# Performance work log

Hardware: AMD Instinct MI355X
Metric: run time of the kernel (lower is better)

Reference implementation:

```python
import jax, jax.numpy as jnp
import numpy as np

N_NODES = 20000
N_EDGES = 320000
BATCH = 8
N_OBS = 6
N_FIXED = 10
HID = 128
N_LAYERS = 3


def setup_inputs() -> dict:
    key = jax.random.key(0)
    ks = jax.random.split(key, 6)
    x = jax.random.normal(ks[0], (BATCH * N_NODES, N_OBS), dtype=jnp.float32)
    fixed_node_features = jax.random.normal(ks[1], (N_NODES, N_FIXED), dtype=jnp.float32)
    edge_index = jax.random.randint(ks[2], (2, N_EDGES), 0, N_NODES)
    W_in = jax.random.normal(ks[3], (N_OBS + N_FIXED, HID), dtype=jnp.float32) * 0.1
    b_in = jnp.zeros((HID,), jnp.float32)
    Wg = jax.random.normal(ks[4], (N_LAYERS, HID, HID), dtype=jnp.float32) * 0.05
    bg = jnp.zeros((N_LAYERS, HID), jnp.float32)
    return {"x": x, "fixed_node_features": fixed_node_features, "W_in": W_in,
            "b_in": b_in, "Wg": Wg, "bg": bg, "edge_index": edge_index}


def reference(x, fixed_node_features, W_in, b_in, Wg, bg, edge_index):
    # GCN normalization with self-loops (PyG gcn_norm defaults):
    self_loops = jnp.arange(N_NODES)
    row = jnp.concatenate([edge_index[0], self_loops])  # source nodes [E+N]
    col = jnp.concatenate([edge_index[1], self_loops])  # target nodes [E+N]
    deg = jax.ops.segment_sum(jnp.ones_like(col, dtype=jnp.float32), col,
                              num_segments=N_NODES)
    dinv = jnp.where(deg > 0, jax.lax.rsqrt(jnp.maximum(deg, 1.0)), 0.0)
    norm = dinv[row] * dinv[col]  # [E+N]

    # input projection: [B*N, n_obs] -> [B, N, n_obs+n_fixed] -> [B, N, H]
    h = x.reshape(BATCH, N_NODES, N_OBS)
    h = jnp.concatenate(
        [h, jnp.broadcast_to(fixed_node_features, (BATCH, N_NODES, N_FIXED))],
        axis=-1)
    h = h @ W_in + b_in

    # stacked GCNConv + ReLU (gather -> normalize -> scatter-add)
    for l in range(N_LAYERS):
        t = h @ Wg[l]                              # [B, N, H]
        msgs = t[:, row, :] * norm[None, :, None]  # [B, E+N, H]
        agg = jnp.zeros_like(t).at[:, col, :].add(msgs)
        h = jax.nn.relu(agg + bg[l])

    return h.reshape(-1, HID)
```

## Files before the change

kernel.cpp:

```cpp
#include <hip/hip_runtime.h>
#include <hip/hip_bf16.h>
#include <cstdint>

#define N_NODES 20000
#define N_EDGES 320000
#define BATCH 8
#define HID 128

static constexpr size_t O_DEG  = 0;
static constexpr size_t O_CUR  = 81920;
static constexpr size_t O_OFF  = 163840;
static constexpr size_t O_DINV = 245760;
static constexpr size_t O_CSR  = 327680;
static constexpr size_t O_CSRW = 1376256;
static constexpr size_t O_P32  = 3473408;
static constexpr size_t O_HBUF = 3553408;


__global__ void count_deg(const int* __restrict__ col, int* __restrict__ deg) {
    int e = blockIdx.x * 256 + threadIdx.x;
    if (e < N_EDGES) atomicAdd(&deg[col[e]], 1);
}

__global__ void compute_dinv(const int* __restrict__ deg, float* __restrict__ dinv) {
    int i = blockIdx.x * 256 + threadIdx.x;
    if (i < N_NODES) {
        float d = (float)(deg[i] + 1);
        dinv[i] = 1.0f / sqrtf(d);
    }
}

__global__ __launch_bounds__(1024) void scan_offsets(const int* __restrict__ deg,
                                                     int* __restrict__ off) {
    __shared__ int part[1024];
    const int CH = 20;
    int tid = threadIdx.x;
    int base = tid * CH;
    int s = 0;
    for (int i = 0; i < CH; ++i) {
        int idx = base + i;
        if (idx < N_NODES) s += (deg[idx] + 7) & ~7;
    }
    part[tid] = s;
    __syncthreads();
    for (int d = 1; d < 1024; d <<= 1) {
        int add = 0;
        if (tid >= d) add = part[tid - d];
        __syncthreads();
        part[tid] += add;
        __syncthreads();
    }
    int run = part[tid] - s;
    for (int i = 0; i < CH; ++i) {
        int idx = base + i;
        if (idx < N_NODES) {
            off[idx] = run;
            run += (deg[idx] + 7) & ~7;
        }
    }
    if (tid == 1023) off[N_NODES] = part[1023];
}

__global__ void fill_csr(const int* __restrict__ rowi, const int* __restrict__ coli,
                         const float* __restrict__ dinv, const int* __restrict__ off,
                         int* __restrict__ cursor, uint16_t* __restrict__ csr,
                         float* __restrict__ csrw) {
    int e = blockIdx.x * 256 + threadIdx.x;
    if (e >= N_EDGES) return;
    int r = rowi[e], c = coli[e];
    int pos = atomicAdd(&cursor[c], 1);
    int i = off[c] + pos;
    csr[i] = (uint16_t)r;
    csrw[i] = dinv[r] * dinv[c];
}

__global__ void pad_csr(const int* __restrict__ deg, const int* __restrict__ off,
                        uint16_t* __restrict__ csr, float* __restrict__ csrw) {
    int n = blockIdx.x * 256 + threadIdx.x;
    if (n >= N_NODES) return;
    int d = deg[n];
    int pd = (d + 7) & ~7;
    int s = off[n];
    uint16_t filler = d > 0 ? csr[s + d - 1] : (uint16_t)n;
    for (int i = d; i < pd; ++i) {
        csr[s + i] = filler;
        csrw[s + i] = 0.0f;
    }
}

__global__ __launch_bounds__(64) void sort_adj(const int* __restrict__ degv,
                                               const int* __restrict__ off,
                                               uint16_t* __restrict__ csr,
                                               float* __restrict__ csrw) {
    int n = blockIdx.x;
    int s = off[n];
    int deg = degv[n];
    if (deg <= 1 || deg > 64) return;
    int l = threadIdx.x;
    int my = (l < deg) ? (int)csr[s + l] : 0x7fffffff;
    float mw = (l < deg) ? csrw[s + l] : 0.0f;
    int rank = 0;
    for (int j = 0; j < deg; ++j) {
        int kj = __shfl(my, j);
        rank += (kj < my) || (kj == my && j < l);
    }
    if (l < deg) { csr[s + rank] = (uint16_t)my; csrw[s + rank] = mw; }
}

__global__ __launch_bounds__(64) void build_perm32(const int* __restrict__ deg,
                                                   int* __restrict__ perm) {
    int tid = threadIdx.x;
    int l = tid & 31;
    int grp = blockIdx.x * 2 + (tid >> 5);
    if (grp >= N_NODES / 32) return;
    int n = grp * 32 + l;
    int key = (deg[n] + 7) & ~7;
    int rank = 0;
    for (int j = 0; j < 32; ++j) {
        int kj = __shfl(key, j, 32);
        rank += (kj < key) || (kj == key && j < l);
    }
    perm[grp * 32 + rank] = n;
}

__global__ __launch_bounds__(256) void input_proj(const float* __restrict__ x,
                                                  const float* __restrict__ fixedf,
                                                  const float* __restrict__ W,
                                                  const float* __restrict__ bvec,
                                                  float* __restrict__ h) {
    __shared__ float Ws[16 * HID];
    __shared__ float xs[BATCH * 6];
    __shared__ float fs[10];
    int n = blockIdx.x, tid = threadIdx.x;
    for (int i = tid; i < 16 * HID; i += 256) Ws[i] = W[i];
    if (tid < 48) {
        int b_ = tid / 6, o = tid % 6;
        xs[tid] = x[((size_t)b_ * N_NODES + n) * 6 + o];
    } else if (tid < 58) {
        fs[tid - 48] = fixedf[(size_t)n * 10 + (tid - 48)];
    }
    __syncthreads();
#pragma unroll
    for (int j = 0; j < 4; ++j) {
        int idx = tid + j * 256;
        int bb = idx >> 7, hh = idx & 127;
        float acc = bvec[hh];
#pragma unroll
        for (int k = 0; k < 6; ++k) acc += xs[bb * 6 + k] * Ws[k * HID + hh];
#pragma unroll
        for (int k = 0; k < 10; ++k) acc += fs[k] * Ws[(6 + k) * HID + hh];
        size_t a = ((size_t)((hh >> 5) * 8 + bb) * N_NODES + n) * 32 + (hh & 31);
        h[a] = acc;
    }
}

__global__ __launch_bounds__(256) void aggregate_xcd(const float* __restrict__ hin,
                                                     const int* __restrict__ off,
                                                     const uint16_t* __restrict__ csr,
                                                     const float* __restrict__ csrw,
                                                     const float* __restrict__ dinv,
                                                     const int* __restrict__ perm,
                                                     float* __restrict__ out,
                                                     int final_scatter) {
    int bid = blockIdx.x;
    int b   = bid & 7;
    int q   = bid / 5000;
    int g   = (bid - q * 5000) >> 3;
    int tid = threadIdx.x;
    int l = tid & 63;
    int n = perm[g * 32 + ((tid >> 6) << 3) + (l >> 3)];
    int sub = l & 7;
    const size_t SB4 = (size_t)(q * 8 + b) * N_NODES * 8;

    const float4* hp4 = (const float4*)hin;
    float dn = dinv[n];
    float d2 = dn * dn;
    float4 acc = hp4[SB4 + (size_t)n * 8 + sub];
    acc.x *= d2; acc.y *= d2; acc.z *= d2; acc.w *= d2;
    float4 acc2 = make_float4(0.f, 0.f, 0.f, 0.f);

    int s = off[n], e = off[n + 1];
    for (int p = s; p < e; p += 8) {
        uint4  iv = *(const uint4*)(csr + p);
        float4 wa = *(const float4*)(csrw + p);
        float4 wb = *(const float4*)(csrw + p + 4);
        int s0 = iv.x & 0xffff, s1 = iv.x >> 16;
        int s2 = iv.y & 0xffff, s3 = iv.y >> 16;
        int s4 = iv.z & 0xffff, s5 = iv.z >> 16;
        int s6 = iv.w & 0xffff, s7 = iv.w >> 16;
        float4 v0 = hp4[SB4 + (size_t)s0 * 8 + sub];
        float4 v1 = hp4[SB4 + (size_t)s1 * 8 + sub];
        float4 v2 = hp4[SB4 + (size_t)s2 * 8 + sub];
        float4 v3 = hp4[SB4 + (size_t)s3 * 8 + sub];
        float4 v4 = hp4[SB4 + (size_t)s4 * 8 + sub];
        float4 v5 = hp4[SB4 + (size_t)s5 * 8 + sub];
        float4 v6 = hp4[SB4 + (size_t)s6 * 8 + sub];
        float4 v7 = hp4[SB4 + (size_t)s7 * 8 + sub];
        acc.x  += wa.x * v0.x + wa.y * v1.x + wa.z * v2.x + wa.w * v3.x;
        acc.y  += wa.x * v0.y + wa.y * v1.y + wa.z * v2.y + wa.w * v3.y;
        acc.z  += wa.x * v0.z + wa.y * v1.z + wa.z * v2.z + wa.w * v3.z;
        acc.w  += wa.x * v0.w + wa.y * v1.w + wa.z * v2.w + wa.w * v3.w;
        acc2.x += wb.x * v4.x + wb.y * v5.x + wb.z * v6.x + wb.w * v7.x;
        acc2.y += wb.x * v4.y + wb.y * v5.y + wb.z * v6.y + wb.w * v7.y;
        acc2.z += wb.x * v4.z + wb.y * v5.z + wb.z * v6.z + wb.w * v7.z;
        acc2.w += wb.x * v4.w + wb.y * v5.w + wb.z * v6.w + wb.w * v7.w;
    }
    acc.x += acc2.x; acc.y += acc2.y; acc.z += acc2.z; acc.w += acc2.w;

    size_t o4 = final_scatter ? ((size_t)(b * N_NODES + n) * 32 + q * 8 + sub)
                              : (SB4 + (size_t)n * 8 + sub);
    ((float4*)out)[o4] = acc;
}

__global__ __launch_bounds__(512, 4) void gemm_bias_relu(const float* __restrict__ in,
                                                         float* __restrict__ outp,
                                                         const float* __restrict__ W,
                                                         const float* __restrict__ bias,
                                                         int dense) {
    __shared__ float As_T[32][260];
    __shared__ float Wls[32][132];
    int tid = threadIdx.x;
    int rg = tid >> 4;
    int cg = tid & 15;
    int b  = blockIdx.x / 79;
    int n0 = (blockIdx.x % 79) * 256;
    float acc[8][8] = {};
    const float4* in4 = (const float4*)in;

    for (int kt = 0; kt < HID; kt += 32) {
        int q = kt >> 5;
        __syncthreads();
#pragma unroll
        for (int i = 0; i < 4; ++i) {
            int f = tid + i * 512;
            int row = f >> 3;
            int kk4 = f & 7;
            int n = n0 + row;
            if (n > N_NODES - 1) n = N_NODES - 1;
            size_t rb4 = dense ? (((size_t)b * N_NODES + n) * 32 + q * 8)
                               : (((size_t)(q * 8 + b) * N_NODES + n) * 8);
            float4 v = in4[rb4 + kk4];
            int kk = kk4 << 2;
            As_T[kk + 0][row] = v.x;
            As_T[kk + 1][row] = v.y;
            As_T[kk + 2][row] = v.z;
            As_T[kk + 3][row] = v.w;
        }
#pragma unroll
        for (int i = 0; i < 2; ++i) {
            int f = tid + i * 512;
            int row = f >> 5;
            int kk = (f & 31) << 2;
            *(float4*)&Wls[row][kk] = *(const float4*)&W[(size_t)(kt + row) * HID + kk];
        }
        __syncthreads();
#pragma unroll 8
        for (int k = 0; k < 32; ++k) {
            float4 a0 = *(const float4*)&As_T[k][rg * 8];
            float4 a1 = *(const float4*)&As_T[k][rg * 8 + 4];
            float4 w0 = *(const float4*)&Wls[k][cg * 4];
            float4 w1 = *(const float4*)&Wls[k][cg * 4 + 64];
            float av[8] = {a0.x, a0.y, a0.z, a0.w, a1.x, a1.y, a1.z, a1.w};
            float wv[8] = {w0.x, w0.y, w0.z, w0.w, w1.x, w1.y, w1.z, w1.w};
#pragma unroll
            for (int i = 0; i < 8; ++i)
#pragma unroll
                for (int j = 0; j < 8; ++j)
                    acc[i][j] += av[i] * wv[j];
        }
    }

    float4 b0 = *(const float4*)&bias[cg * 4];
    float4 b1 = *(const float4*)&bias[cg * 4 + 64];
    float4* out4 = (float4*)outp;
#pragma unroll
    for (int i = 0; i < 8; ++i) {
        int n = n0 + rg * 8 + i;
        if (n >= N_NODES) break;
        float4 o0, o1;
        o0.x = fmaxf(acc[i][0] + b0.x, 0.0f);
        o0.y = fmaxf(acc[i][1] + b0.y, 0.0f);
        o0.z = fmaxf(acc[i][2] + b0.z, 0.0f);
        o0.w = fmaxf(acc[i][3] + b0.w, 0.0f);
        o1.x = fmaxf(acc[i][4] + b1.x, 0.0f);
        o1.y = fmaxf(acc[i][5] + b1.y, 0.0f);
        o1.z = fmaxf(acc[i][6] + b1.z, 0.0f);
        o1.w = fmaxf(acc[i][7] + b1.w, 0.0f);
        if (dense) {
            size_t r4 = ((size_t)b * N_NODES + n) * 32;
            out4[r4 + cg] = o0;
            out4[r4 + cg + 16] = o1;
        } else {
            int q0 = cg >> 3, f0 = cg & 7;
            out4[((size_t)(q0 * 8 + b) * N_NODES + n) * 8 + f0] = o0;
            out4[((size_t)((q0 + 2) * 8 + b) * N_NODES + n) * 8 + f0] = o1;
        }
    }
}

extern "C" void kernel_launch(void* const* d_in, const int* in_sizes, int n_in,
                              void* d_out, int out_size, void* d_ws, size_t ws_size,
                              hipStream_t stream) {
    const float* x      = (const float*)d_in[0];
    const float* fixedf = (const float*)d_in[1];
    const float* W_in   = (const float*)d_in[2];
    const float* b_in   = (const float*)d_in[3];
    const float* Wg     = (const float*)d_in[4];
    const float* bg     = (const float*)d_in[5];
    const int*   ei     = (const int*)d_in[6];

    const int* rowi = ei;
    const int* coli = ei + N_EDGES;

    char* ws = (char*)d_ws;
    int*      deg    = (int*)(ws + O_DEG);
    int*      cursor = (int*)(ws + O_CUR);
    int*      off    = (int*)(ws + O_OFF);
    float*    dinv   = (float*)(ws + O_DINV);
    uint16_t* csr    = (uint16_t*)(ws + O_CSR);
    float*    csrw   = (float*)(ws + O_CSRW);
    int*      perm   = (int*)(ws + O_P32);
    float*    hA     = (float*)(ws + O_HBUF);
    float*    hB     = (float*)d_out;

    hipMemsetAsync(deg, 0, N_NODES * sizeof(int), stream);
    hipMemsetAsync(cursor, 0, N_NODES * sizeof(int), stream);

    count_deg<<<(N_EDGES + 255) / 256, 256, 0, stream>>>(coli, deg);
    compute_dinv<<<(N_NODES + 255) / 256, 256, 0, stream>>>(deg, dinv);
    scan_offsets<<<1, 1024, 0, stream>>>(deg, off);
    fill_csr<<<(N_EDGES + 255) / 256, 256, 0, stream>>>(rowi, coli, dinv, off, cursor,
                                                        csr, csrw);
    pad_csr<<<(N_NODES + 255) / 256, 256, 0, stream>>>(deg, off, csr, csrw);
    sort_adj<<<N_NODES, 64, 0, stream>>>(deg, off, csr, csrw);
    build_perm32<<<(N_NODES / 32 + 1) / 2, 64, 0, stream>>>(deg, perm);

    input_proj<<<N_NODES, 256, 0, stream>>>(x, fixedf, W_in, b_in, hA);

    const int AB = 4 * 5000;
    const int GB = 8 * 79;

    aggregate_xcd<<<AB, 256, 0, stream>>>(hA, off, csr, csrw, dinv, perm, hB, 0);
    gemm_bias_relu<<<GB, 512, 0, stream>>>(hB, hB, Wg + 0 * HID * HID, bg + 0 * HID, 0);
    aggregate_xcd<<<AB, 256, 0, stream>>>(hB, off, csr, csrw, dinv, perm, hA, 0);
    gemm_bias_relu<<<GB, 512, 0, stream>>>(hA, hA, Wg + 1 * HID * HID, bg + 1 * HID, 0);
    aggregate_xcd<<<AB, 256, 0, stream>>>(hA, off, csr, csrw, dinv, perm, (float*)d_out, 1);
    gemm_bias_relu<<<GB, 512, 0, stream>>>((float*)d_out, (float*)d_out,
                                           Wg + 2 * HID * HID, bg + 2 * HID, 1);
}
```

Before: 627.8 us.

## Drop per-edge weight array and compute GCN norm from dinv on the fly

```diff
diff --git a/kernel.cpp b/kernel.cpp
--- a/kernel.cpp
+++ b/kernel.cpp
@@ -12,9 +12,8 @@
 static constexpr size_t O_OFF  = 163840;
 static constexpr size_t O_DINV = 245760;
 static constexpr size_t O_CSR  = 327680;
-static constexpr size_t O_CSRW = 1376256;
-static constexpr size_t O_P32  = 3473408;
-static constexpr size_t O_HBUF = 3553408;
+static constexpr size_t O_P32  = 1376256;
+static constexpr size_t O_HBUF = 1458176;
 
 
 __global__ void count_deg(const int* __restrict__ col, int* __restrict__ deg) {
@@ -62,49 +61,41 @@
 }
 
 __global__ void fill_csr(const int* __restrict__ rowi, const int* __restrict__ coli,
-                         const float* __restrict__ dinv, const int* __restrict__ off,
-                         int* __restrict__ cursor, uint16_t* __restrict__ csr,
-                         float* __restrict__ csrw) {
+                         const int* __restrict__ off, int* __restrict__ cursor,
+                         uint16_t* __restrict__ csr) {
     int e = blockIdx.x * 256 + threadIdx.x;
     if (e >= N_EDGES) return;
     int r = rowi[e], c = coli[e];
     int pos = atomicAdd(&cursor[c], 1);
-    int i = off[c] + pos;
-    csr[i] = (uint16_t)r;
-    csrw[i] = dinv[r] * dinv[c];
+    csr[off[c] + pos] = (uint16_t)r;
 }
 
 __global__ void pad_csr(const int* __restrict__ deg, const int* __restrict__ off,
-                        uint16_t* __restrict__ csr, float* __restrict__ csrw) {
+                        uint16_t* __restrict__ csr) {
     int n = blockIdx.x * 256 + threadIdx.x;
     if (n >= N_NODES) return;
     int d = deg[n];
     int pd = (d + 7) & ~7;
     int s = off[n];
     uint16_t filler = d > 0 ? csr[s + d - 1] : (uint16_t)n;
-    for (int i = d; i < pd; ++i) {
-        csr[s + i] = filler;
-        csrw[s + i] = 0.0f;
-    }
+    for (int i = d; i < pd; ++i) csr[s + i] = filler;
 }
 
 __global__ __launch_bounds__(64) void sort_adj(const int* __restrict__ degv,
                                                const int* __restrict__ off,
-                                               uint16_t* __restrict__ csr,
-                                               float* __restrict__ csrw) {
+                                               uint16_t* __restrict__ csr) {
     int n = blockIdx.x;
     int s = off[n];
     int deg = degv[n];
     if (deg <= 1 || deg > 64) return;
     int l = threadIdx.x;
     int my = (l < deg) ? (int)csr[s + l] : 0x7fffffff;
-    float mw = (l < deg) ? csrw[s + l] : 0.0f;
     int rank = 0;
     for (int j = 0; j < deg; ++j) {
         int kj = __shfl(my, j);
         rank += (kj < my) || (kj == my && j < l);
     }
-    if (l < deg) { csr[s + rank] = (uint16_t)my; csrw[s + rank] = mw; }
+    if (l < deg) csr[s + rank] = (uint16_t)my;
 }
 
 __global__ __launch_bounds__(64) void build_perm32(const int* __restrict__ deg,
@@ -157,7 +148,7 @@
 __global__ __launch_bounds__(256) void aggregate_xcd(const float* __restrict__ hin,
                                                      const int* __restrict__ off,
                                                      const uint16_t* __restrict__ csr,
-                                                     const float* __restrict__ csrw,
+                                                     const int* __restrict__ degv,
                                                      const float* __restrict__ dinv,
                                                      const int* __restrict__ perm,
                                                      float* __restrict__ out,
@@ -174,20 +165,30 @@
 
     const float4* hp4 = (const float4*)hin;
     float dn = dinv[n];
-    float d2 = dn * dn;
-    float4 acc = hp4[SB4 + (size_t)n * 8 + sub];
-    acc.x *= d2; acc.y *= d2; acc.z *= d2; acc.w *= d2;
+    float4 vs = hp4[SB4 + (size_t)n * 8 + sub];
+    float4 acc = make_float4(dn * vs.x, dn * vs.y, dn * vs.z, dn * vs.w);
     float4 acc2 = make_float4(0.f, 0.f, 0.f, 0.f);
 
     int s = off[n], e = off[n + 1];
+    int re = s + degv[n];
     for (int p = s; p < e; p += 8) {
         uint4  iv = *(const uint4*)(csr + p);
-        float4 wa = *(const float4*)(csrw + p);
-        float4 wb = *(const float4*)(csrw + p + 4);
         int s0 = iv.x & 0xffff, s1 = iv.x >> 16;
         int s2 = iv.y & 0xffff, s3 = iv.y >> 16;
         int s4 = iv.z & 0xffff, s5 = iv.z >> 16;
         int s6 = iv.w & 0xffff, s7 = iv.w >> 16;
+        float w0 = dinv[s0], w1 = dinv[s1], w2 = dinv[s2], w3 = dinv[s3];
+        float w4 = dinv[s4], w5 = dinv[s5], w6 = dinv[s6], w7 = dinv[s7];
+        if (p + 8 > re) {
+            w0 = (p + 0 < re) ? w0 : 0.f;
+            w1 = (p + 1 < re) ? w1 : 0.f;
+            w2 = (p + 2 < re) ? w2 : 0.f;
+            w3 = (p + 3 < re) ? w3 : 0.f;
+            w4 = (p + 4 < re) ? w4 : 0.f;
+            w5 = (p + 5 < re) ? w5 : 0.f;
+            w6 = (p + 6 < re) ? w6 : 0.f;
+            w7 = (p + 7 < re) ? w7 : 0.f;
+        }
         float4 v0 = hp4[SB4 + (size_t)s0 * 8 + sub];
         float4 v1 = hp4[SB4 + (size_t)s1 * 8 + sub];
         float4 v2 = hp4[SB4 + (size_t)s2 * 8 + sub];
@@ -196,34 +197,37 @@
         float4 v5 = hp4[SB4 + (size_t)s5 * 8 + sub];
         float4 v6 = hp4[SB4 + (size_t)s6 * 8 + sub];
         float4 v7 = hp4[SB4 + (size_t)s7 * 8 + sub];
-        acc.x  += wa.x * v0.x + wa.y * v1.x + wa.z * v2.x + wa.w * v3.x;
-        acc.y  += wa.x * v0.y + wa.y * v1.y + wa.z * v2.y + wa.w * v3.y;
-        acc.z  += wa.x * v0.z + wa.y * v1.z + wa.z * v2.z + wa.w * v3.z;
-        acc.w  += wa.x * v0.w + wa.y * v1.w + wa.z * v2.w + wa.w * v3.w;
-        acc2.x += wb.x * v4.x + wb.y * v5.x + wb.z * v6.x + wb.w * v7.x;
-        acc2.y += wb.x * v4.y + wb.y * v5.y + wb.z * v6.y + wb.w * v7.y;
-        acc2.z += wb.x * v4.z + wb.y * v5.z + wb.z * v6.z + wb.w * v7.z;
-        acc2.w += wb.x * v4.w + wb.y * v5.w + wb.z * v6.w + wb.w * v7.w;
-    }
-    acc.x += acc2.x; acc.y += acc2.y; acc.z += acc2.z; acc.w += acc2.w;
+        acc.x  += w0 * v0.x + w1 * v1.x + w2 * v2.x + w3 * v3.x;
+        acc.y  += w0 * v0.y + w1 * v1.y + w2 * v2.y + w3 * v3.y;
+        acc.z  += w0 * v0.z + w1 * v1.z + w2 * v2.z + w3 * v3.z;
+        acc.w  += w0 * v0.w + w1 * v1.w + w2 * v2.w + w3 * v3.w;
+        acc2.x += w4 * v4.x + w5 * v5.x + w6 * v6.x + w7 * v7.x;
+        acc2.y += w4 * v4.y + w5 * v5.y + w6 * v6.y + w7 * v7.y;
+        acc2.z += w4 * v4.z + w5 * v5.z + w6 * v6.z + w7 * v7.z;
+        acc2.w += w4 * v4.w + w5 * v5.w + w6 * v6.w + w7 * v7.w;
+    }
+    acc.x = dn * (acc.x + acc2.x);
+    acc.y = dn * (acc.y + acc2.y);
+    acc.z = dn * (acc.z + acc2.z);
+    acc.w = dn * (acc.w + acc2.w);
 
     size_t o4 = final_scatter ? ((size_t)(b * N_NODES + n) * 32 + q * 8 + sub)
                               : (SB4 + (size_t)n * 8 + sub);
     ((float4*)out)[o4] = acc;
 }
 
-__global__ __launch_bounds__(512, 4) void gemm_bias_relu(const float* __restrict__ in,
-                                                         float* __restrict__ outp,
-                                                         const float* __restrict__ W,
-                                                         const float* __restrict__ bias,
-                                                         int dense) {
-    __shared__ float As_T[32][260];
-    __shared__ float Wls[32][132];
+__global__ __launch_bounds__(256) void gemm_bias_relu(const float* __restrict__ in,
+                                                      float* __restrict__ outp,
+                                                      const float* __restrict__ W,
+                                                      const float* __restrict__ bias,
+                                                      int dense) {
+    __shared__ float As_T[32][132];
+    __shared__ float Wls[32][HID];
     int tid = threadIdx.x;
     int rg = tid >> 4;
     int cg = tid & 15;
-    int b  = blockIdx.x / 79;
-    int n0 = (blockIdx.x % 79) * 256;
+    int b  = blockIdx.x & 7;
+    int n0 = (blockIdx.x >> 3) * 128;
     float acc[8][8] = {};
     const float4* in4 = (const float4*)in;
 
@@ -232,7 +236,7 @@
         __syncthreads();
 #pragma unroll
         for (int i = 0; i < 4; ++i) {
-            int f = tid + i * 512;
+            int f = tid + i * 256;
             int row = f >> 3;
             int kk4 = f & 7;
             int n = n0 + row;
@@ -247,8 +251,8 @@
             As_T[kk + 3][row] = v.w;
         }
 #pragma unroll
-        for (int i = 0; i < 2; ++i) {
-            int f = tid + i * 512;
+        for (int i = 0; i < 4; ++i) {
+            int f = tid + i * 256;
             int row = f >> 5;
             int kk = (f & 31) << 2;
             *(float4*)&Wls[row][kk] = *(const float4*)&W[(size_t)(kt + row) * HID + kk];
@@ -318,7 +322,6 @@
     int*      off    = (int*)(ws + O_OFF);
     float*    dinv   = (float*)(ws + O_DINV);
     uint16_t* csr    = (uint16_t*)(ws + O_CSR);
-    float*    csrw   = (float*)(ws + O_CSRW);
     int*      perm   = (int*)(ws + O_P32);
     float*    hA     = (float*)(ws + O_HBUF);
     float*    hB     = (float*)d_out;
@@ -329,22 +332,21 @@
     count_deg<<<(N_EDGES + 255) / 256, 256, 0, stream>>>(coli, deg);
     compute_dinv<<<(N_NODES + 255) / 256, 256, 0, stream>>>(deg, dinv);
     scan_offsets<<<1, 1024, 0, stream>>>(deg, off);
-    fill_csr<<<(N_EDGES + 255) / 256, 256, 0, stream>>>(rowi, coli, dinv, off, cursor,
-                                                        csr, csrw);
-    pad_csr<<<(N_NODES + 255) / 256, 256, 0, stream>>>(deg, off, csr, csrw);
-    sort_adj<<<N_NODES, 64, 0, stream>>>(deg, off, csr, csrw);
+    fill_csr<<<(N_EDGES + 255) / 256, 256, 0, stream>>>(rowi, coli, off, cursor, csr);
+    pad_csr<<<(N_NODES + 255) / 256, 256, 0, stream>>>(deg, off, csr);
+    sort_adj<<<N_NODES, 64, 0, stream>>>(deg, off, csr);
     build_perm32<<<(N_NODES / 32 + 1) / 2, 64, 0, stream>>>(deg, perm);
 
     input_proj<<<N_NODES, 256, 0, stream>>>(x, fixedf, W_in, b_in, hA);
 
     const int AB = 4 * 5000;
-    const int GB = 8 * 79;
-
-    aggregate_xcd<<<AB, 256, 0, stream>>>(hA, off, csr, csrw, dinv, perm, hB, 0);
-    gemm_bias_relu<<<GB, 512, 0, stream>>>(hB, hB, Wg + 0 * HID * HID, bg + 0 * HID, 0);
-    aggregate_xcd<<<AB, 256, 0, stream>>>(hB, off, csr, csrw, dinv, perm, hA, 0);
-    gemm_bias_relu<<<GB, 512, 0, stream>>>(hA, hA, Wg + 1 * HID * HID, bg + 1 * HID, 0);
-    aggregate_xcd<<<AB, 256, 0, stream>>>(hA, off, csr, csrw, dinv, perm, (float*)d_out, 1);
-    gemm_bias_relu<<<GB, 512, 0, stream>>>((float*)d_out, (float*)d_out,
+    const int GB = 157 * 8;
+
+    aggregate_xcd<<<AB, 256, 0, stream>>>(hA, off, csr, deg, dinv, perm, hB, 0);
+    gemm_bias_relu<<<GB, 256, 0, stream>>>(hB, hB, Wg + 0 * HID * HID, bg + 0 * HID, 0);
+    aggregate_xcd<<<AB, 256, 0, stream>>>(hB, off, csr, deg, dinv, perm, hA, 0);
+    gemm_bias_relu<<<GB, 256, 0, stream>>>(hA, hA, Wg + 1 * HID * HID, bg + 1 * HID, 0);
+    aggregate_xcd<<<AB, 256, 0, stream>>>(hA, off, csr, deg, dinv, perm, (float*)d_out, 1);
+    gemm_bias_relu<<<GB, 256, 0, stream>>>((float*)d_out, (float*)d_out,
                                            Wg + 2 * HID * HID, bg + 2 * HID, 1);
 }
```

Measured after the change: 628.1 us. Within noise of the previous version (+0.0%).
